# Kernel optimization log

Hardware: AMD Instinct MI355X
Metric: run time of the kernel (lower is better)

## Reference

```python
import jax, jax.numpy as jnp
import numpy as np

EPS = 1e-5
F_BIAS = 1.0
KEEP_H = 0.7
KEEP_C = 0.7


def _block_layernorm(x, gamma, beta, n_blocks, h):
    # Normalize each of the n_blocks chunks of width h independently,
    # then apply a single per-feature gain/bias of size n_blocks*h.
    B = x.shape[0]
    xb = x.reshape(B, n_blocks, h)
    mean = jnp.mean(xb, axis=-1, keepdims=True)
    var = jnp.mean(jnp.square(xb - mean), axis=-1, keepdims=True)
    xn = (xb - mean) * jax.lax.rsqrt(var + EPS)
    return xn.reshape(B, n_blocks * h) * gamma + beta


def setup_inputs() -> dict:
    key = jax.random.key(0)
    ks = jax.random.split(key, 7)
    B, X, H = 65536, 256, 256
    x = jax.random.normal(ks[0], (B, X), dtype=jnp.float32)
    h = jax.random.normal(ks[1], (B, H), dtype=jnp.float32)
    c = jax.random.normal(ks[2], (B, H), dtype=jnp.float32)
    # orthogonal-initializer stand-in: scaled gaussian
    W_full = jax.random.normal(ks[3], (X + H, 4 * H), dtype=jnp.float32) / np.sqrt(X + H)
    bias = jnp.zeros((4 * H,), dtype=jnp.float32)
    g1 = jnp.ones((4 * H,), dtype=jnp.float32)
    b1 = jnp.zeros((4 * H,), dtype=jnp.float32)
    g2 = jnp.ones((H,), dtype=jnp.float32)
    b2 = jnp.zeros((H,), dtype=jnp.float32)
    mask_h = jax.random.uniform(ks[4], (B, H), dtype=jnp.float32)
    mask_c = jax.random.uniform(ks[5], (B, H), dtype=jnp.float32)
    return {"x": x, "h": h, "c": c, "W_full": W_full, "bias": bias,
            "g1": g1, "b1": b1, "g2": g2, "b2": b2,
            "mask_h": mask_h, "mask_c": mask_c}


def reference(x, h, c, W_full, bias, g1, b1, g2, b2, mask_h, mask_c):
    H = h.shape[1]
    concat = jnp.concatenate([x, h], axis=1) @ W_full + bias       # [B, 4H]
    concat = _block_layernorm(concat, g1, b1, 4, H)
    i, j, f, o = jnp.split(concat, 4, axis=1)
    new_c = c * jax.nn.sigmoid(f + F_BIAS) + jax.nn.sigmoid(i) * jnp.tanh(j)
    new_c = _block_layernorm(new_c, g2, b2, 1, H)
    new_h = jnp.tanh(new_c) * jax.nn.sigmoid(o)
    # zoneout: keep the NEW state with prob keep, else carry over old state
    mh = (mask_h < KEEP_H).astype(new_h.dtype)
    mc = (mask_c < KEEP_C).astype(new_c.dtype)
    new_h = mh * new_h + (1.0 - mh) * h
    new_c = mc * new_c + (1.0 - mc) * c
    return (new_h, new_c)
```

## Files before the change

kernel.cpp:

```cpp
#include <hip/hip_runtime.h>


#define NTHREADS 512
#define TILE_M 64
#define PRE_STRIDE 20

typedef _Float16 half8 __attribute__((ext_vector_type(8)));
typedef _Float16 half4v __attribute__((ext_vector_type(4)));
typedef float float4v __attribute__((ext_vector_type(4)));

__device__ __forceinline__ void async16(const void* g, void* l) {
  __builtin_amdgcn_global_load_lds(
      (const __attribute__((address_space(1))) unsigned int*)g,
      (__attribute__((address_space(3))) unsigned int*)l, 16, 0, 0);
}

__device__ __forceinline__ float sigm(float x) {
  return __fdividef(1.0f, 1.0f + __expf(-x));
}
__device__ __forceinline__ float tanh_fast(float x) {
  return 2.0f * __fdividef(1.0f, 1.0f + __expf(-2.0f * x)) - 1.0f;
}

__global__ __launch_bounds__(256) void wt_kernel(const float* __restrict__ W,
                                                 _Float16* __restrict__ Wt) {
  __shared__ float tile[64][65];
  const int bn = blockIdx.x << 6;
  const int bk = blockIdx.y << 6;
  const int tid = threadIdx.x;
#pragma unroll
  for (int i = 0; i < 16; ++i) {
    int idx = (i << 8) + tid;
    int kk = idx >> 6, nn = idx & 63;
    tile[kk][nn] = W[(size_t)(bk + kk) * 1024 + bn + nn];
  }
  __syncthreads();
#pragma unroll
  for (int i = 0; i < 16; ++i) {
    int idx = (i << 8) + tid;
    int nn = idx >> 6, kk = idx & 63;
    Wt[(size_t)(bn + nn) * 512 + bk + kk] = (_Float16)tile[kk][nn];
  }
}

__global__ __launch_bounds__(NTHREADS, 2) void lstm_fused(
    const float* __restrict__ x, const float* __restrict__ hin,
    const float* __restrict__ cin, const _Float16* __restrict__ Wt,
    const float* __restrict__ bias, const float* __restrict__ g1,
    const float* __restrict__ b1, const float* __restrict__ g2,
    const float* __restrict__ b2, const float* __restrict__ mhp,
    const float* __restrict__ mcp, float* __restrict__ out) {
  extern __shared__ char smem[];
  _Float16* aT = (_Float16*)smem;
  _Float16* wTh = (_Float16*)(smem + 4096);
  _Float16* preT = (_Float16*)smem;

  const int tid = threadIdx.x;
  const int wave = tid >> 6;
  const int lane = tid & 63;
  const int l15 = lane & 15;
  const int quad = lane >> 4;
  const int blockRow = blockIdx.x * TILE_M;

  float4v acc[4][8];
#pragma unroll
  for (int s = 0; s < 4; ++s)
#pragma unroll
    for (int c = 0; c < 8; ++c) acc[s][c] = (float4v){0.f, 0.f, 0.f, 0.f};

  const int arow = tid >> 3;
  const int ap4 = (tid & 7) << 2;
  const float* xrow = x + (size_t)(blockRow + arow) * 256 + ap4;
  const float* hrow = hin + (size_t)(blockRow + arow) * 256 + ap4;
  _Float16* adst = aT + arow * 32 + (((ap4 >> 3) ^ (arow & 3)) << 3) + (ap4 & 4);

  const int wnl0 = tid >> 2;
  const int wj = (tid & 3) ^ (wnl0 & 3);
  const char* wg = (const char*)Wt + (size_t)wnl0 * 1024 + wj * 16;
  char* wl = (char*)wTh + tid * 16;

  const int aslot = quad ^ (l15 & 3);

  for (int iter = 0; iter < 16; ++iter) {
    {
      const float* src = (iter < 8) ? (xrow + iter * 32) : (hrow + (iter - 8) * 32);
      float4 v = *(const float4*)src;
      half4v hv = {(_Float16)v.x, (_Float16)v.y, (_Float16)v.z, (_Float16)v.w};
      *(half4v*)adst = hv;
    }
#pragma unroll
    for (int it = 0; it < 4; ++it)
      async16(wg + it * 131072 + iter * 64, wl + it * 8192);
    __syncthreads();

    half8 af[4];
#pragma unroll
    for (int s = 0; s < 4; ++s)
      af[s] = *(const half8*)(aT + (s * 16 + l15) * 32 + aslot * 8);
    {
      half8 bf[4];
#pragma unroll
      for (int cc = 0; cc < 4; ++cc) {
        int nl = wave * 64 + cc * 16 + l15;
        bf[cc] = *(const half8*)(wTh + nl * 32 + aslot * 8);
      }
#pragma unroll
      for (int s = 0; s < 4; ++s)
#pragma unroll
        for (int cc = 0; cc < 4; ++cc)
          acc[s][cc] = __builtin_amdgcn_mfma_f32_16x16x32_f16(af[s], bf[cc], acc[s][cc], 0, 0, 0);
    }
    __syncthreads();
#pragma unroll
    for (int it = 0; it < 4; ++it)
      async16(wg + 524288 + it * 131072 + iter * 64, wl + it * 8192);
    __syncthreads();
    {
      half8 bf[4];
#pragma unroll
      for (int cc = 0; cc < 4; ++cc) {
        int nl = wave * 64 + cc * 16 + l15;
        bf[cc] = *(const half8*)(wTh + nl * 32 + aslot * 8);
      }
#pragma unroll
      for (int s = 0; s < 4; ++s)
#pragma unroll
        for (int cc = 0; cc < 4; ++cc)
          acc[s][4 + cc] =
              __builtin_amdgcn_mfma_f32_16x16x32_f16(af[s], bf[cc], acc[s][4 + cc], 0, 0, 0);
    }
    __syncthreads();
  }

  float* out_h = out;
  float* out_c = out + (size_t)65536 * 256;
  const int er = tid >> 5;
  const int et = tid & 31;

#pragma unroll
  for (int p = 0; p < 4; ++p) {
    __syncthreads();
#pragma unroll
    for (int c = 0; c < 8; ++c) {
      int n = ((c >> 2) << 9) + wave * 64 + ((c & 3) << 4) + l15;
      float4v a = acc[p][c];
      half4v hv = {(_Float16)a.x, (_Float16)a.y, (_Float16)a.z, (_Float16)a.w};
      *(half4v*)(preT + n * PRE_STRIDE + (quad << 2)) = hv;
    }
    __syncthreads();

    const int rg = blockRow + (p << 4) + er;
    float mean1[4], rstd1[4];
#pragma unroll
    for (int ch = 0; ch < 4; ++ch) {
      float s = 0.f, q = 0.f;
#pragma unroll
      for (int ss = 0; ss < 8; ++ss) {
        int n = (ch << 8) + (ss << 5) + et;
        float v = (float)preT[n * PRE_STRIDE + er] + bias[n];
        s += v;
        q += v * v;
      }
#pragma unroll
      for (int m = 1; m < 32; m <<= 1) {
        s += __shfl_xor(s, m, 32);
        q += __shfl_xor(q, m, 32);
      }
      float mu = s * (1.0f / 256.0f);
      mean1[ch] = mu;
      rstd1[ch] = __frsqrt_rn(q * (1.0f / 256.0f) - mu * mu + 1e-5f);
    }

    float ncp[8], so[8], cv[8];
    float s2 = 0.f, q2 = 0.f;
#pragma unroll
    for (int ss = 0; ss < 8; ++ss) {
      int hc = (ss << 5) + et;
      float iv = ((float)preT[(hc)*PRE_STRIDE + er] + bias[hc] - mean1[0]) * rstd1[0] * g1[hc] + b1[hc];
      float jv = ((float)preT[(256 + hc) * PRE_STRIDE + er] + bias[256 + hc] - mean1[1]) * rstd1[1] * g1[256 + hc] + b1[256 + hc];
      float fv = ((float)preT[(512 + hc) * PRE_STRIDE + er] + bias[512 + hc] - mean1[2]) * rstd1[2] * g1[512 + hc] + b1[512 + hc];
      float ov = ((float)preT[(768 + hc) * PRE_STRIDE + er] + bias[768 + hc] - mean1[3]) * rstd1[3] * g1[768 + hc] + b1[768 + hc];
      float cval = cin[(size_t)rg * 256 + hc];
      float nc = cval * sigm(fv + 1.0f) + sigm(iv) * tanh_fast(jv);
      ncp[ss] = nc;
      so[ss] = sigm(ov);
      cv[ss] = cval;
      s2 += nc;
      q2 += nc * nc;
    }
#pragma unroll
    for (int m = 1; m < 32; m <<= 1) {
      s2 += __shfl_xor(s2, m, 32);
      q2 += __shfl_xor(q2, m, 32);
    }
    float mu2 = s2 * (1.0f / 256.0f);
    float rstd2 = __frsqrt_rn(q2 * (1.0f / 256.0f) - mu2 * mu2 + 1e-5f);
#pragma unroll
    for (int ss = 0; ss < 8; ++ss) {
      int hc = (ss << 5) + et;
      size_t gi = (size_t)rg * 256 + hc;
      float ncn = (ncp[ss] - mu2) * rstd2 * g2[hc] + b2[hc];
      float nh = tanh_fast(ncn) * so[ss];
      float hval = hin[gi];
      out_h[gi] = (mhp[gi] < 0.7f) ? nh : hval;
      out_c[gi] = (mcp[gi] < 0.7f) ? ncn : cv[ss];
    }
  }
}

extern "C" void kernel_launch(void* const* d_in, const int* in_sizes, int n_in,
                              void* d_out, int out_size, void* d_ws, size_t ws_size,
                              hipStream_t stream) {
  (void)in_sizes; (void)n_in; (void)out_size; (void)ws_size;
  const float* x = (const float*)d_in[0];
  const float* h = (const float*)d_in[1];
  const float* c = (const float*)d_in[2];
  const float* W = (const float*)d_in[3];
  const float* bias = (const float*)d_in[4];
  const float* g1 = (const float*)d_in[5];
  const float* b1 = (const float*)d_in[6];
  const float* g2 = (const float*)d_in[7];
  const float* b2 = (const float*)d_in[8];
  const float* mh = (const float*)d_in[9];
  const float* mc = (const float*)d_in[10];
  _Float16* Wt = (_Float16*)d_ws;

  wt_kernel<<<dim3(16, 8), dim3(256), 0, stream>>>(W, Wt);
  lstm_fused<<<dim3(1024), dim3(NTHREADS), 40960, stream>>>(
      x, h, c, Wt, bias, g1, b1, g2, b2, mh, mc, (float*)d_out);
}
```

Baseline: 508.8 us.

## Load GEMM operands directly to registers with prefetch, drop LDS staging

Drops the LDS staging of the activation and weight tiles in the GEMM main loop. Each lane now loads its MFMA fragments straight from global memory into registers, and the next k-step's operands are software-prefetched while the current MFMAs run. This removes four __syncthreads per iteration and the LDS round trips. The cost is uncoalesced or duplicated global loads, since each row of A is loaded separately by every wave, and extra registers that could reduce occupancy at the launch bound of two blocks.

```diff
diff --git a/kernel.cpp b/kernel.cpp
--- a/kernel.cpp
+++ b/kernel.cpp
@@ -8,12 +8,6 @@
 typedef _Float16 half8 __attribute__((ext_vector_type(8)));
 typedef _Float16 half4v __attribute__((ext_vector_type(4)));
 typedef float float4v __attribute__((ext_vector_type(4)));
-
-__device__ __forceinline__ void async16(const void* g, void* l) {
-  __builtin_amdgcn_global_load_lds(
-      (const __attribute__((address_space(1))) unsigned int*)g,
-      (__attribute__((address_space(3))) unsigned int*)l, 16, 0, 0);
-}
 
 __device__ __forceinline__ float sigm(float x) {
   return __fdividef(1.0f, 1.0f + __expf(-x));
@@ -51,8 +45,6 @@
     const float* __restrict__ b2, const float* __restrict__ mhp,
     const float* __restrict__ mcp, float* __restrict__ out) {
   extern __shared__ char smem[];
-  _Float16* aT = (_Float16*)smem;
-  _Float16* wTh = (_Float16*)(smem + 4096);
   _Float16* preT = (_Float16*)smem;
 
   const int tid = threadIdx.x;
@@ -68,68 +60,70 @@
 #pragma unroll
     for (int c = 0; c < 8; ++c) acc[s][c] = (float4v){0.f, 0.f, 0.f, 0.f};
 
-  const int arow = tid >> 3;
-  const int ap4 = (tid & 7) << 2;
-  const float* xrow = x + (size_t)(blockRow + arow) * 256 + ap4;
-  const float* hrow = hin + (size_t)(blockRow + arow) * 256 + ap4;
-  _Float16* adst = aT + arow * 32 + (((ap4 >> 3) ^ (arow & 3)) << 3) + (ap4 & 4);
-
-  const int wnl0 = tid >> 2;
-  const int wj = (tid & 3) ^ (wnl0 & 3);
-  const char* wg = (const char*)Wt + (size_t)wnl0 * 1024 + wj * 16;
-  char* wl = (char*)wTh + tid * 16;
-
-  const int aslot = quad ^ (l15 & 3);
+  const float* xb = x + (size_t)blockRow * 256;
+  const float* hb = hin + (size_t)blockRow * 256;
+
+  int aoff[4];
+#pragma unroll
+  for (int s = 0; s < 4; ++s) aoff[s] = (s * 16 + l15) * 256 + quad * 8;
+  int wofs[8];
+#pragma unroll
+  for (int cc = 0; cc < 8; ++cc) {
+    int col = ((cc >> 2) << 9) + wave * 64 + ((cc & 3) << 4) + l15;
+    wofs[cc] = col * 512 + quad * 8;
+  }
+
+  float4v a0[4], a1[4];
+  half8 wn[8];
+
+#pragma unroll
+  for (int s = 0; s < 4; ++s) {
+    const float* p = xb + aoff[s];
+    a0[s] = *(const float4v*)p;
+    a1[s] = *(const float4v*)(p + 4);
+  }
+#pragma unroll
+  for (int cc = 0; cc < 8; ++cc) wn[cc] = *(const half8*)(Wt + wofs[cc]);
 
   for (int iter = 0; iter < 16; ++iter) {
-    {
-      const float* src = (iter < 8) ? (xrow + iter * 32) : (hrow + (iter - 8) * 32);
-      float4 v = *(const float4*)src;
-      half4v hv = {(_Float16)v.x, (_Float16)v.y, (_Float16)v.z, (_Float16)v.w};
-      *(half4v*)adst = hv;
-    }
-#pragma unroll
-    for (int it = 0; it < 4; ++it)
-      async16(wg + it * 131072 + iter * 64, wl + it * 8192);
-    __syncthreads();
-
     half8 af[4];
 #pragma unroll
     for (int s = 0; s < 4; ++s)
-      af[s] = *(const half8*)(aT + (s * 16 + l15) * 32 + aslot * 8);
-    {
-      half8 bf[4];
-#pragma unroll
-      for (int cc = 0; cc < 4; ++cc) {
-        int nl = wave * 64 + cc * 16 + l15;
-        bf[cc] = *(const half8*)(wTh + nl * 32 + aslot * 8);
+      af[s] = (half8){(_Float16)a0[s].x, (_Float16)a0[s].y, (_Float16)a0[s].z,
+                      (_Float16)a0[s].w, (_Float16)a1[s].x, (_Float16)a1[s].y,
+                      (_Float16)a1[s].z, (_Float16)a1[s].w};
+    const int ni = iter + 1;
+    const bool more = ni < 16;
+    if (more) {
+      const float* base = (ni < 8) ? xb : hb;
+      const int ko = (ni & 7) << 5;
+#pragma unroll
+      for (int s = 0; s < 4; ++s) {
+        const float* p = base + aoff[s] + ko;
+        a0[s] = *(const float4v*)p;
+        a1[s] = *(const float4v*)(p + 4);
       }
-#pragma unroll
-      for (int s = 0; s < 4; ++s)
-#pragma unroll
-        for (int cc = 0; cc < 4; ++cc)
-          acc[s][cc] = __builtin_amdgcn_mfma_f32_16x16x32_f16(af[s], bf[cc], acc[s][cc], 0, 0, 0);
-    }
-    __syncthreads();
-#pragma unroll
-    for (int it = 0; it < 4; ++it)
-      async16(wg + 524288 + it * 131072 + iter * 64, wl + it * 8192);
-    __syncthreads();
-    {
-      half8 bf[4];
-#pragma unroll
-      for (int cc = 0; cc < 4; ++cc) {
-        int nl = wave * 64 + cc * 16 + l15;
-        bf[cc] = *(const half8*)(wTh + nl * 32 + aslot * 8);
-      }
-#pragma unroll
-      for (int s = 0; s < 4; ++s)
-#pragma unroll
-        for (int cc = 0; cc < 4; ++cc)
-          acc[s][4 + cc] =
-              __builtin_amdgcn_mfma_f32_16x16x32_f16(af[s], bf[cc], acc[s][4 + cc], 0, 0, 0);
-    }
-    __syncthreads();
+    }
+#pragma unroll
+    for (int s = 0; s < 4; ++s)
+#pragma unroll
+      for (int cc = 0; cc < 4; ++cc)
+        acc[s][cc] = __builtin_amdgcn_mfma_f32_16x16x32_f16(af[s], wn[cc], acc[s][cc], 0, 0, 0);
+    if (more) {
+#pragma unroll
+      for (int cc = 0; cc < 4; ++cc)
+        wn[cc] = *(const half8*)(Wt + wofs[cc] + ni * 32);
+    }
+#pragma unroll
+    for (int s = 0; s < 4; ++s)
+#pragma unroll
+      for (int cc = 4; cc < 8; ++cc)
+        acc[s][cc] = __builtin_amdgcn_mfma_f32_16x16x32_f16(af[s], wn[cc], acc[s][cc], 0, 0, 0);
+    if (more) {
+#pragma unroll
+      for (int cc = 4; cc < 8; ++cc)
+        wn[cc] = *(const half8*)(Wt + wofs[cc] + ni * 32);
+    }
   }
 
   float* out_h = out;
```

Result: slower. 625.3 us (+22.9%).
